# Performance work log

Measured on AMD Instinct MI355X. Metric: run time of the kernel, lower is better.

Reference implementation:

```python
import jax, jax.numpy as jnp
import numpy as np

ITEMNUM = 50000
NUM_HEADS = 4
EPS = 1e-8


def _ln(x, g, b):
    m = x.mean(-1, keepdims=True)
    v = ((x - m) ** 2).mean(-1, keepdims=True)
    return (x - m) * jax.lax.rsqrt(v + EPS) * g + b


def _forward(seqs_data, position, seqs, time_emb, pos_table, gate_W, gate_b,
             ln_attn_g, ln_attn_b, qW, qb, kW, kb, vW, vb,
             ln_ffn_g, ln_ffn_b, c1W, c1b, c2W, c2b, last_g, last_b):
    B, L, H = seqs.shape
    nb = qW.shape[0]
    hd = H // NUM_HEADS

    pe = pos_table[position]                      # [B,L,H]
    seqs = seqs + pe
    time = time_emb + pe
    # per-position per-block time gates, [B,L,nb]
    gates = jax.nn.sigmoid(jnp.einsum('blh,nh->bln', time, gate_W) + gate_b)

    keep = (seqs_data != ITEMNUM - 1)[..., None].astype(seqs.dtype)  # [B,L,1]
    seqs = seqs * keep
    tril = jnp.tril(jnp.ones((L, L), dtype=bool))  # causal: keep lower triangle
    neg_inf = jnp.asarray(-jnp.inf, seqs.dtype)
    scale = 1.0 / np.sqrt(hd).astype(np.float32)

    for i in range(nb):
        Q = _ln(seqs, ln_attn_g[i], ln_attn_b[i])
        q = Q @ qW[i].T + qb[i]
        k = time @ kW[i].T + kb[i]
        v = (seqs + time) @ vW[i].T + vb[i]
        # [B,nh,L,hd]
        q = q.reshape(B, L, NUM_HEADS, hd).transpose(0, 2, 1, 3)
        k = k.reshape(B, L, NUM_HEADS, hd).transpose(0, 2, 1, 3)
        v = v.reshape(B, L, NUM_HEADS, hd).transpose(0, 2, 1, 3)
        scores = jnp.einsum('bhqd,bhkd->bhqk', q, k) * scale  # [B,nh,L,L]
        tg = gates[:, :, i]                                   # [B,L]
        gate_mat = tg[:, None, :, None] * tg[:, None, None, :]  # [B,1,L,L] outer product
        scores = jnp.where(tril[None, None], scores * gate_mat, neg_inf)
        attn = jax.nn.softmax(scores, axis=-1)
        out = jnp.einsum('bhqk,bhkd->bhqd', attn, v)
        out = out.transpose(0, 2, 1, 3).reshape(B, L, H)
        x = Q + out
        x = _ln(x, ln_ffn_g[i], ln_ffn_b[i])
        # PointWiseFeedForward: two 1x1 convs == two linears, relu, residual
        h = jax.nn.relu(x @ c1W[i].T + c1b[i])
        seqs = (h @ c2W[i].T + c2b[i] + x) * keep

    return _ln(seqs, last_g, last_b)


def setup_inputs() -> dict:
    key = jax.random.key(0)
    B, L, H, NB, ML = 64, 512, 256, 2, 512
    ks = iter(jax.random.split(key, 32))
    nrm = lambda shape, s=0.05: jax.random.normal(next(ks), shape, jnp.float32) * s
    pos_table = nrm((ML, H), 0.02).at[0].set(0.0)  # padding_idx=0
    inp = {
        'seqs_data': jax.random.randint(next(ks), (B, L), 0, ITEMNUM - 1, jnp.int32),
        'seqs': nrm((B, L, H), 1.0),
        'position': jax.random.randint(next(ks), (B, L), 0, ML, jnp.int32),
        'time_emb': nrm((B, L, H), 1.0),
        'pos_table': pos_table,
        'gate_W': nrm((NB, H)), 'gate_b': jnp.zeros((NB,), jnp.float32),
        'ln_attn_g': jnp.ones((NB, H), jnp.float32), 'ln_attn_b': jnp.zeros((NB, H), jnp.float32),
        'qW': nrm((NB, H, H)), 'qb': jnp.zeros((NB, H), jnp.float32),
        'kW': nrm((NB, H, H)), 'kb': jnp.zeros((NB, H), jnp.float32),
        'vW': nrm((NB, H, H)), 'vb': jnp.zeros((NB, H), jnp.float32),
        'ln_ffn_g': jnp.ones((NB, H), jnp.float32), 'ln_ffn_b': jnp.zeros((NB, H), jnp.float32),
        'c1W': nrm((NB, H, H)), 'c1b': jnp.zeros((NB, H), jnp.float32),
        'c2W': nrm((NB, H, H)), 'c2b': jnp.zeros((NB, H), jnp.float32),
        'last_g': jnp.ones((H,), jnp.float32), 'last_b': jnp.zeros((H,), jnp.float32),
    }
    return inp


def reference(seqs_data, seqs, position, time_emb, pos_table, gate_W, gate_b,
              ln_attn_g, ln_attn_b, qW, qb, kW, kb, vW, vb,
              ln_ffn_g, ln_ffn_b, c1W, c1b, c2W, c2b, last_g, last_b):
    return _forward(seqs_data, position, seqs, time_emb, pos_table, gate_W, gate_b,
                    ln_attn_g, ln_attn_b, qW, qb, kW, kb, vW, vb,
                    ln_ffn_g, ln_ffn_b, c1W, c1b, c2W, c2b, last_g, last_b)
```

## Files before the change

### kernel.cpp

```cpp
#include <hip/hip_runtime.h>
#include <hip/hip_bf16.h>
#include <math.h>

#define NTOK 32768
#define Hdim 256
#define Ldim 512
#define Bdim 64
#define NHEAD 4
#define HD 64
#define PADV 49999

typedef __bf16 bf16x8 __attribute__((ext_vector_type(8)));
typedef __bf16 bf16x4 __attribute__((ext_vector_type(4)));
typedef float  f32x4  __attribute__((ext_vector_type(4)));
typedef unsigned short u16x8 __attribute__((ext_vector_type(8)));

union bf8u { bf16x8 v8; bf16x4 v4[2]; };

__device__ __forceinline__ unsigned short f2bf(float f) {
    unsigned int u = __float_as_uint(f);
    unsigned int r = (u + 0x7fffu + ((u >> 16) & 1u)) >> 16;
    return (unsigned short)r;
}
__device__ __forceinline__ float bf2f(unsigned short u) {
    return __uint_as_float(((unsigned int)u) << 16);
}

__device__ __forceinline__ void gload16(const void* g, void* l) {
    __builtin_amdgcn_global_load_lds((const __attribute__((address_space(1))) unsigned int*)g,
                                     (__attribute__((address_space(3))) unsigned int*)l,
                                     16, 0, 0);
}

__global__ __launch_bounds__(256)
void castw_kernel(const float* __restrict__ q, const float* __restrict__ k,
                  const float* __restrict__ v, const float* __restrict__ c1,
                  const float* __restrict__ c2, unsigned short* __restrict__ dst) {
    const float* srcs[5] = {q, k, v, c1, c2};
    const float* s = srcs[blockIdx.y];
    int idx = blockIdx.x * 1024 + threadIdx.x * 4;
    float4 f = *(const float4*)(s + idx);
    unsigned short* d = dst + (size_t)blockIdx.y * 131072 + idx;
    d[0] = f2bf(f.x); d[1] = f2bf(f.y); d[2] = f2bf(f.z); d[3] = f2bf(f.w);
}

__global__ __launch_bounds__(256)
void prep_ln_kernel(const int* __restrict__ seqs_data, const float* __restrict__ seqs,
                    const int* __restrict__ position, const float* __restrict__ time_emb,
                    const float* __restrict__ pos_table, const float* __restrict__ gate_W,
                    const float* __restrict__ gate_b,
                    const float* __restrict__ lnG, const float* __restrict__ lnB,
                    unsigned short* __restrict__ Tbf,
                    unsigned short* __restrict__ QXbf,
                    unsigned short* __restrict__ VINbf,
                    float* __restrict__ gates, float* __restrict__ keepv) {
    int tok  = blockIdx.x * 4 + (threadIdx.x >> 6);
    int lane = threadIdx.x & 63;
    size_t off = (size_t)tok * Hdim + lane * 4;
    int pos = position[tok];
    float4 pe = *(const float4*)(pos_table + (size_t)pos * Hdim + lane * 4);
    float4 sq = *(const float4*)(seqs + off);
    float4 tm = *(const float4*)(time_emb + off);
    float keep = (seqs_data[tok] != PADV) ? 1.0f : 0.0f;
    float4 t = {tm.x + pe.x, tm.y + pe.y, tm.z + pe.z, tm.w + pe.w};
    float4 s = {(sq.x + pe.x) * keep, (sq.y + pe.y) * keep,
                (sq.z + pe.z) * keep, (sq.w + pe.w) * keep};
    ushort4 tb = {f2bf(t.x), f2bf(t.y), f2bf(t.z), f2bf(t.w)};
    *(ushort4*)(Tbf + off) = tb;
    float4 gw0 = *(const float4*)(gate_W + lane * 4);
    float4 gw1 = *(const float4*)(gate_W + Hdim + lane * 4);
    float r0 = s.x + s.y + s.z + s.w;
    float r1 = s.x * s.x + s.y * s.y + s.z * s.z + s.w * s.w;
    float r2 = t.x * gw0.x + t.y * gw0.y + t.z * gw0.z + t.w * gw0.w;
    float r3 = t.x * gw1.x + t.y * gw1.y + t.z * gw1.z + t.w * gw1.w;
#pragma unroll
    for (int o = 1; o < 64; o <<= 1) {
        r0 += __shfl_xor(r0, o, 64);
        r1 += __shfl_xor(r1, o, 64);
        r2 += __shfl_xor(r2, o, 64);
        r3 += __shfl_xor(r3, o, 64);
    }
    float mean = r0 * (1.0f / Hdim);
    float var  = fmaxf(r1 * (1.0f / Hdim) - mean * mean, 0.0f);
    float rstd = rsqrtf(var + 1e-8f);
    if (lane == 0) {
        gates[(size_t)tok * 2 + 0] = 1.0f / (1.0f + __expf(-(r2 + gate_b[0])));
        gates[(size_t)tok * 2 + 1] = 1.0f / (1.0f + __expf(-(r3 + gate_b[1])));
        keepv[tok] = keep;
    }
    float4 g4 = *(const float4*)(lnG + lane * 4);
    float4 b4 = *(const float4*)(lnB + lane * 4);
    float4 y = {(s.x - mean) * rstd * g4.x + b4.x, (s.y - mean) * rstd * g4.y + b4.y,
                (s.z - mean) * rstd * g4.z + b4.z, (s.w - mean) * rstd * g4.w + b4.w};
    ushort4 yb = {f2bf(y.x), f2bf(y.y), f2bf(y.z), f2bf(y.w)};
    *(ushort4*)(QXbf + off) = yb;
    ushort4 vb = {f2bf(s.x + t.x), f2bf(s.y + t.y), f2bf(s.z + t.z), f2bf(s.w + t.w)};
    *(ushort4*)(VINbf + off) = vb;
}

#define GBM 128
#define GBN 128
#define GBK 64

__device__ __forceinline__ void stage64(const unsigned short* __restrict__ src,
                                        size_t rowBase, __bf16* lds, int tid, int kc) {
#pragma unroll
    for (int it = 0; it < 4; ++it) {
        int c = tid + it * 256;
        int r = c >> 3, sub = c & 7;
        int g = sub ^ (r & 7);
        gload16(src + (rowBase + r) * Hdim + kc + g * 8, lds + c * 8);
    }
}
__device__ __forceinline__ bf16x8 frag64(const __bf16* lds, int r, int g) {
    return *(const bf16x8*)(lds + r * 64 + (g ^ (r & 7)) * 8);
}

__global__ __launch_bounds__(256)
void gemm_qkv_kernel(const unsigned short* __restrict__ QXbf,
                     const unsigned short* __restrict__ Tbf,
                     const unsigned short* __restrict__ VINbf,
                     const unsigned short* __restrict__ qW,
                     const unsigned short* __restrict__ kW,
                     const unsigned short* __restrict__ vW,
                     const float* __restrict__ qb, const float* __restrict__ kb,
                     const float* __restrict__ vb,
                     unsigned short* __restrict__ Qbf,
                     unsigned short* __restrict__ Kbf,
                     unsigned short* __restrict__ VT) {
    __shared__ __align__(16) char smem[128 * 136 * 2];
    __bf16* As = (__bf16*)smem;
    __bf16* Ws = (__bf16*)(smem + 16384);
    __bf16 (*Ct)[136] = (__bf16 (*)[136])smem;
    int z = blockIdx.z;
    const unsigned short* A = (z == 0) ? QXbf : (z == 1) ? Tbf : VINbf;
    const unsigned short* W = (z == 0) ? qW : (z == 1) ? kW : vW;
    const float* bias       = (z == 0) ? qb : (z == 1) ? kb : vb;

    int tid = threadIdx.x, lane = tid & 63, w = tid >> 6;
    int wr = w >> 1, wc = w & 1;
    int m0 = blockIdx.y * GBM, n0 = blockIdx.x * GBN;
    f32x4 acc[4][4];
#pragma unroll
    for (int i = 0; i < 4; ++i)
#pragma unroll
        for (int j = 0; j < 4; ++j) acc[i][j] = (f32x4)(0.0f);
    int colq = lane & 15, kg = lane >> 4;
    for (int kc = 0; kc < Hdim; kc += GBK) {
        __syncthreads();
        stage64(A, m0, As, tid, kc);
        stage64(W, n0, Ws, tid, kc);
        __syncthreads();
        bf16x8 af[4][2], bfr[4][2];
#pragma unroll
        for (int i = 0; i < 4; ++i) {
            int r = wr * 64 + i * 16 + colq;
            af[i][0] = frag64(As, r, kg);
            af[i][1] = frag64(As, r, 4 + kg);
        }
#pragma unroll
        for (int j = 0; j < 4; ++j) {
            int r = wc * 64 + j * 16 + colq;
            bfr[j][0] = frag64(Ws, r, kg);
            bfr[j][1] = frag64(Ws, r, 4 + kg);
        }
#pragma unroll
        for (int i = 0; i < 4; ++i)
#pragma unroll
            for (int j = 0; j < 4; ++j) {
                acc[i][j] = __builtin_amdgcn_mfma_f32_16x16x32_bf16(af[i][0], bfr[j][0], acc[i][j], 0, 0, 0);
                acc[i][j] = __builtin_amdgcn_mfma_f32_16x16x32_bf16(af[i][1], bfr[j][1], acc[i][j], 0, 0, 0);
            }
    }
    int rowq = (lane >> 4) * 4;
    if (z < 2) {
        unsigned short* outBF = (z == 0) ? Qbf : Kbf;
#pragma unroll
        for (int i = 0; i < 4; ++i)
#pragma unroll
            for (int r = 0; r < 4; ++r) {
                int m = m0 + wr * 64 + i * 16 + rowq + r;
#pragma unroll
                for (int j = 0; j < 4; ++j) {
                    int n = n0 + wc * 64 + j * 16 + colq;
                    outBF[(size_t)m * Hdim + n] = f2bf(acc[i][j][r] + bias[n]);
                }
            }
    } else {
        __syncthreads();
#pragma unroll
        for (int i = 0; i < 4; ++i)
#pragma unroll
            for (int r = 0; r < 4; ++r) {
                int ml = wr * 64 + i * 16 + rowq + r;
#pragma unroll
                for (int j = 0; j < 4; ++j) {
                    int nl = wc * 64 + j * 16 + colq;
                    Ct[nl][ml] = (__bf16)(acc[i][j][r] + bias[n0 + nl]);
                }
            }
        __syncthreads();
        int bb = m0 >> 9, l0 = m0 & 511;
#pragma unroll
        for (int it = 0; it < 8; ++it) {
            int c = tid + it * 256;
            int nl = c >> 4;
            int o8 = (c & 15) * 8;
            int n = n0 + nl;
            int hh = n >> 6, dd = n & 63;
            bf16x8 v = *(const bf16x8*)&Ct[nl][o8];
            *(bf16x8*)(VT + ((((size_t)bb * NHEAD + hh) * HD + dd) * Ldim + l0 + o8)) = v;
        }
    }
}

#define FFN_LDS (65536 + 32768)

__device__ __forceinline__ int swz(int r, int g) {
    return (g & 24) | ((g & 7) ^ (r & 7));
}

__device__ __forceinline__ void ffn_gemm(const unsigned short* __restrict__ W,
                                         const __bf16* Abuf, __bf16* Wst,
                                         int tid, int wr, int wc, int colq, int kg,
                                         f32x4 acc[4][4]) {
#pragma unroll
    for (int i = 0; i < 4; ++i)
#pragma unroll
        for (int j = 0; j < 4; ++j) acc[i][j] = (f32x4)(0.0f);
    for (int kc = 0; kc < Hdim; kc += 64) {
        __syncthreads();
#pragma unroll
        for (int it = 0; it < 4; ++it) {
            int c = tid + it * 512;
            int r = c >> 3, sub = c & 7;
            int g = sub ^ (r & 7);
            gload16(W + (size_t)r * Hdim + kc + g * 8, Wst + c * 8);
        }
        __syncthreads();
        bf16x8 af[4][2], bfr[4][2];
#pragma unroll
        for (int i = 0; i < 4; ++i) {
            int r = wr * 64 + i * 16 + colq;
            af[i][0] = *(const bf16x8*)(Abuf + r * 256 + kc + ((kg) ^ (r & 7)) * 8);
            af[i][1] = *(const bf16x8*)(Abuf + r * 256 + kc + ((4 + kg) ^ (r & 7)) * 8);
        }
#pragma unroll
        for (int j = 0; j < 4; ++j) {
            int n = wc * 64 + j * 16 + colq;
            bfr[j][0] = frag64(Wst, n, kg);
            bfr[j][1] = frag64(Wst, n, 4 + kg);
        }
#pragma unroll
        for (int i = 0; i < 4; ++i)
#pragma unroll
            for (int j = 0; j < 4; ++j) {
                acc[i][j] = __builtin_amdgcn_mfma_f32_16x16x32_bf16(af[i][0], bfr[j][0], acc[i][j], 0, 0, 0);
                acc[i][j] = __builtin_amdgcn_mfma_f32_16x16x32_bf16(af[i][1], bfr[j][1], acc[i][j], 0, 0, 0);
            }
    }
}

__global__ __launch_bounds__(512, 1)
void ffn_kernel(const unsigned short* __restrict__ Qx,
                const unsigned short* __restrict__ Qa,
                const float* __restrict__ lnG, const float* __restrict__ lnB,
                const unsigned short* __restrict__ c1Wb, const float* __restrict__ c1b,
                const unsigned short* __restrict__ c2Wb, const float* __restrict__ c2b,
                const float* __restrict__ keepv,
                const unsigned short* __restrict__ Tbf,
                const float* __restrict__ oG, const float* __restrict__ oB,
                float* __restrict__ outF,
                unsigned short* __restrict__ QxOut,
                unsigned short* __restrict__ VINout) {
    extern __shared__ __align__(16) char smem[];
    __bf16* Abuf   = (__bf16*)smem;
    __bf16* Wst    = (__bf16*)(smem + 65536);
    float*  statsF = (float*)(smem + 65536);

    int m0  = blockIdx.x * 128;
    int tid = threadIdx.x, lane = tid & 63, w = tid >> 6;
    int wr = w >> 2, wc = w & 3;
    int colq = lane & 15, kg = lane >> 4;
    int rowq = (lane >> 4) * 4;

    float xc[8][8];
#pragma unroll
    for (int it = 0; it < 8; ++it) {
        int c = tid + it * 512;
        int r = c >> 5, g = c & 31;
        size_t off = (size_t)(m0 + r) * Hdim + g * 8;
        u16x8 qv = *(const u16x8*)(Qx + off);
        u16x8 av = *(const u16x8*)(Qa + off);
        float cs = 0.0f, cq = 0.0f;
#pragma unroll
        for (int j = 0; j < 8; ++j) {
            float x = bf2f(qv[j]) + bf2f(av[j]);
            xc[it][j] = x;
            cs += x; cq += x * x;
        }
#pragma unroll
        for (int o = 1; o < 32; o <<= 1) {
            cs += __shfl_xor(cs, o, 32);
            cq += __shfl_xor(cq, o, 32);
        }
        if ((tid & 31) == 0) { statsF[r * 2] = cs; statsF[r * 2 + 1] = cq; }
    }
    __syncthreads();
    u16x8 xnreg[8];
#pragma unroll
    for (int it = 0; it < 8; ++it) {
        int c = tid + it * 512;
        int r = c >> 5, g = c & 31, col = g * 8;
        float mean = statsF[r * 2] * (1.0f / Hdim);
        float var  = fmaxf(statsF[r * 2 + 1] * (1.0f / Hdim) - mean * mean, 0.0f);
        float rstd = rsqrtf(var + 1e-8f);
        float4 g0 = *(const float4*)(lnG + col), g1 = *(const float4*)(lnG + col + 4);
        float4 b0 = *(const float4*)(lnB + col), b1 = *(const float4*)(lnB + col + 4);
        float gv[8] = {g0.x, g0.y, g0.z, g0.w, g1.x, g1.y, g1.z, g1.w};
        float bv[8] = {b0.x, b0.y, b0.z, b0.w, b1.x, b1.y, b1.z, b1.w};
        u16x8 xn;
#pragma unroll
        for (int j = 0; j < 8; ++j)
            xn[j] = f2bf((xc[it][j] - mean) * rstd * gv[j] + bv[j]);
        xnreg[it] = xn;
        *(u16x8*)(Abuf + r * 256 + swz(r, g) * 8) = xn;
    }

    f32x4 acc[4][4];
    ffn_gemm(c1Wb, Abuf, Wst, tid, wr, wc, colq, kg, acc);
    float bj[4];
#pragma unroll
    for (int j = 0; j < 4; ++j) bj[j] = c1b[wc * 64 + j * 16 + colq];
    __syncthreads();
#pragma unroll
    for (int i = 0; i < 4; ++i)
#pragma unroll
        for (int r = 0; r < 4; ++r) {
            int m = wr * 64 + i * 16 + rowq + r;
#pragma unroll
            for (int j = 0; j < 4; ++j) {
                int n = wc * 64 + j * 16 + colq;
                float v = fmaxf(acc[i][j][r] + bj[j], 0.0f);
                Abuf[m * 256 + swz(m, n >> 3) * 8 + (n & 7)] = (__bf16)v;
            }
        }

    ffn_gemm(c2Wb, Abuf, Wst, tid, wr, wc, colq, kg, acc);
#pragma unroll
    for (int j = 0; j < 4; ++j) bj[j] = c2b[wc * 64 + j * 16 + colq];
    __syncthreads();
#pragma unroll
    for (int i = 0; i < 4; ++i)
#pragma unroll
        for (int r = 0; r < 4; ++r) {
            int m = wr * 64 + i * 16 + rowq + r;
#pragma unroll
            for (int j = 0; j < 4; ++j) {
                int n = wc * 64 + j * 16 + colq;
                Abuf[m * 256 + swz(m, n >> 3) * 8 + (n & 7)] = (__bf16)(acc[i][j][r] + bj[j]);
            }
        }
    __syncthreads();

    float sc[8][8];
#pragma unroll
    for (int it = 0; it < 8; ++it) {
        int c = tid + it * 512;
        int r = c >> 5, g = c & 31;
        u16x8 zv = *(const u16x8*)(Abuf + r * 256 + swz(r, g) * 8);
        u16x8 xn = xnreg[it];
        float kf = keepv[m0 + r];
        float cs = 0.0f, cq = 0.0f;
#pragma unroll
        for (int j = 0; j < 8; ++j) {
            float s = (bf2f(zv[j]) + bf2f(xn[j])) * kf;
            sc[it][j] = s;
            cs += s; cq += s * s;
        }
#pragma unroll
        for (int o = 1; o < 32; o <<= 1) {
            cs += __shfl_xor(cs, o, 32);
            cq += __shfl_xor(cq, o, 32);
        }
        if ((tid & 31) == 0) { statsF[r * 2] = cs; statsF[r * 2 + 1] = cq; }
    }
    __syncthreads();
#pragma unroll
    for (int it = 0; it < 8; ++it) {
        int c = tid + it * 512;
        int r = c >> 5, g = c & 31, col = g * 8;
        float mean = statsF[r * 2] * (1.0f / Hdim);
        float var  = fmaxf(statsF[r * 2 + 1] * (1.0f / Hdim) - mean * mean, 0.0f);
        float rstd = rsqrtf(var + 1e-8f);
        float4 g0 = *(const float4*)(oG + col), g1 = *(const float4*)(oG + col + 4);
        float4 b0 = *(const float4*)(oB + col), b1 = *(const float4*)(oB + col + 4);
        float gv[8] = {g0.x, g0.y, g0.z, g0.w, g1.x, g1.y, g1.z, g1.w};
        float bv[8] = {b0.x, b0.y, b0.z, b0.w, b1.x, b1.y, b1.z, b1.w};
        size_t off = (size_t)(m0 + r) * Hdim + col;
        float y[8];
#pragma unroll
        for (int j = 0; j < 8; ++j)
            y[j] = (sc[it][j] - mean) * rstd * gv[j] + bv[j];
        if (outF) {
            float4 o0 = {y[0], y[1], y[2], y[3]};
            float4 o1 = {y[4], y[5], y[6], y[7]};
            *(float4*)(outF + off)     = o0;
            *(float4*)(outF + off + 4) = o1;
        } else {
            u16x8 yb, vb;
            u16x8 tv = *(const u16x8*)(Tbf + off);
#pragma unroll
            for (int j = 0; j < 8; ++j) {
                yb[j] = f2bf(y[j]);
                vb[j] = f2bf(sc[it][j] + bf2f(tv[j]));
            }
            *(u16x8*)(QxOut + off)  = yb;
            *(u16x8*)(VINout + off) = vb;
        }
    }
}

#define AKS 68
#define AVS 516
#define APS 68
#define ATTN_LDS (512 * AKS * 2 + 64 * AVS * 2 + 192 * APS * 2)
__global__ __launch_bounds__(768, 1)
void attn_mfma_kernel(const unsigned short* __restrict__ Qg,
                      const unsigned short* __restrict__ Kg,
                      const unsigned short* __restrict__ VTg,
                      const float* __restrict__ gates,
                      unsigned short* __restrict__ Ob, int blk) {
    extern __shared__ __align__(16) char smem[];
    __bf16 (*Ks)[AKS]  = (__bf16 (*)[AKS])smem;
    __bf16 (*VTs)[AVS] = (__bf16 (*)[AVS])(smem + 512 * AKS * 2);
    __bf16 (*Ps)[APS]  = (__bf16 (*)[APS])(smem + 512 * AKS * 2 + 64 * AVS * 2);
    int h = blockIdx.x & 3, b = blockIdx.x >> 2;
    int tid = threadIdx.x, lane = tid & 63, w = tid >> 6;
    int colq = lane & 15, grp = lane >> 4;
    int rowq = grp * 4, kq = grp * 8;

    size_t baseK = (size_t)b * Ldim * Hdim + h * HD;
    for (int c = tid; c < 4096; c += 768) {
        int r = c >> 3, o = (c & 7) * 8;
        bf8u u;
        u.v8 = *(const bf16x8*)(Kg + baseK + (size_t)r * Hdim + o);
        *(bf16x4*)&Ks[r][o]     = u.v4[0];
        *(bf16x4*)&Ks[r][o + 4] = u.v4[1];
    }
    size_t baseV = ((size_t)b * NHEAD + h) * HD * Ldim;
    for (int c = tid; c < 4096; c += 768) {
        int d = c >> 6, k = (c & 63) * 8;
        bf8u u;
        u.v8 = *(const bf16x8*)(VTg + baseV + (size_t)d * Ldim + k);
        *(bf16x4*)&VTs[d][k]     = u.v4[0];
        *(bf16x4*)&VTs[d][k + 4] = u.v4[1];
    }
    __syncthreads();

    const float lscale = 0.125f * 1.44269504f;
    int gl[3], ng;
    if (w < 4)      { gl[0] = w;     gl[1] = 8 + w;  gl[2] = 28 + w; ng = 3; }
    else if (w < 8) { gl[0] = w;     gl[1] = 8 + w;  gl[2] = 16 + w; ng = 3; }
    else            { gl[0] = 8 + w; gl[1] = 16 + w; gl[2] = 0;      ng = 2; }

    for (int gi = 0; gi < ng; ++gi) {
        int g = gl[gi];
        int q0 = g * 16;
        size_t qrow = (size_t)(b * Ldim + q0 + colq) * Hdim + h * HD;
        bf16x8 afq0 = *(const bf16x8*)(Qg + qrow + kq);
        bf16x8 afq1 = *(const bf16x8*)(Qg + qrow + 32 + kq);
        float gql[4];
#pragma unroll
        for (int r = 0; r < 4; ++r)
            gql[r] = gates[((size_t)b * Ldim + q0 + rowq + r) * 2 + blk] * lscale;

        float lrun[4] = {0.0f, 0.0f, 0.0f, 0.0f};
        f32x4 accO[4];
#pragma unroll
        for (int jd = 0; jd < 4; ++jd) accO[jd] = (f32x4)(0.0f);

        int nfull = g >> 2;
        for (int kt = 0; kt <= nfull; ++kt) {
            int k0 = kt * 64;
            bool diag = (kt == nfull);
            f32x4 sv[4];
#pragma unroll
            for (int j = 0; j < 4; ++j) sv[j] = (f32x4)(0.0f);
#pragma unroll
            for (int j = 0; j < 4; ++j) {
                int kr = k0 + j * 16 + colq;
                bf8u b0, b1;
                b0.v4[0] = *(const bf16x4*)&Ks[kr][kq];
                b0.v4[1] = *(const bf16x4*)&Ks[kr][kq + 4];
                b1.v4[0] = *(const bf16x4*)&Ks[kr][32 + kq];
                b1.v4[1] = *(const bf16x4*)&Ks[kr][32 + kq + 4];
                sv[j] = __builtin_amdgcn_mfma_f32_16x16x32_bf16(afq0, b0.v8, sv[j], 0, 0, 0);
                sv[j] = __builtin_amdgcn_mfma_f32_16x16x32_bf16(afq1, b1.v8, sv[j], 0, 0, 0);
            }
            float gkv[4];
#pragma unroll
            for (int j = 0; j < 4; ++j)
                gkv[j] = gates[((size_t)b * Ldim + k0 + j * 16 + colq) * 2 + blk];
#pragma unroll
            for (int r = 0; r < 4; ++r) {
                float su = 0.0f;
                float p4[4];
                if (diag) {
                    int qg = q0 + rowq + r;
#pragma unroll
                    for (int j = 0; j < 4; ++j) {
                        float v = sv[j][r] * gql[r] * gkv[j];
                        v = (k0 + j * 16 + colq > qg) ? -1e38f : v;
                        float e = exp2f(v);
                        p4[j] = e;
                        su += e;
                    }
                } else {
#pragma unroll
                    for (int j = 0; j < 4; ++j) {
                        float e = exp2f(sv[j][r] * gql[r] * gkv[j]);
                        p4[j] = e;
                        su += e;
                    }
                }
#pragma unroll
                for (int off = 1; off < 16; off <<= 1)
                    su += __shfl_xor(su, off, 16);
                lrun[r] += su;
#pragma unroll
                for (int j = 0; j < 4; ++j)
                    Ps[w * 16 + rowq + r][j * 16 + colq] = (__bf16)p4[j];
            }
            bf8u a0, a1;
            a0.v4[0] = *(const bf16x4*)&Ps[w * 16 + colq][kq];
            a0.v4[1] = *(const bf16x4*)&Ps[w * 16 + colq][kq + 4];
            a1.v4[0] = *(const bf16x4*)&Ps[w * 16 + colq][32 + kq];
            a1.v4[1] = *(const bf16x4*)&Ps[w * 16 + colq][32 + kq + 4];
#pragma unroll
            for (int jd = 0; jd < 4; ++jd) {
                int vr = jd * 16 + colq;
                bf8u v0, v1;
                v0.v4[0] = *(const bf16x4*)&VTs[vr][k0 + kq];
                v0.v4[1] = *(const bf16x4*)&VTs[vr][k0 + kq + 4];
                v1.v4[0] = *(const bf16x4*)&VTs[vr][k0 + 32 + kq];
                v1.v4[1] = *(const bf16x4*)&VTs[vr][k0 + 32 + kq + 4];
                accO[jd] = __builtin_amdgcn_mfma_f32_16x16x32_bf16(a0.v8, v0.v8, accO[jd], 0, 0, 0);
                accO[jd] = __builtin_amdgcn_mfma_f32_16x16x32_bf16(a1.v8, v1.v8, accO[jd], 0, 0, 0);
            }
        }
#pragma unroll
        for (int r = 0; r < 4; ++r) {
            float inv = 1.0f / lrun[r];
#pragma unroll
            for (int jd = 0; jd < 4; ++jd)
                Ob[(size_t)(b * Ldim + q0 + rowq + r) * Hdim + h * HD + jd * 16 + colq] =
                    f2bf(accO[jd][r] * inv);
        }
    }
}

extern "C" void kernel_launch(void* const* d_in, const int* in_sizes, int n_in,
                              void* d_out, int out_size, void* d_ws, size_t ws_size,
                              hipStream_t stream) {
    const int*   seqs_data = (const int*)d_in[0];
    const float* seqs      = (const float*)d_in[1];
    const int*   position  = (const int*)d_in[2];
    const float* time_emb  = (const float*)d_in[3];
    const float* pos_table = (const float*)d_in[4];
    const float* gate_W    = (const float*)d_in[5];
    const float* gate_b    = (const float*)d_in[6];
    const float* ln_attn_g = (const float*)d_in[7];
    const float* ln_attn_b = (const float*)d_in[8];
    const float* qW        = (const float*)d_in[9];
    const float* qb        = (const float*)d_in[10];
    const float* kW        = (const float*)d_in[11];
    const float* kb        = (const float*)d_in[12];
    const float* vW        = (const float*)d_in[13];
    const float* vb        = (const float*)d_in[14];
    const float* ln_ffn_g  = (const float*)d_in[15];
    const float* ln_ffn_b  = (const float*)d_in[16];
    const float* c1W       = (const float*)d_in[17];
    const float* c1b       = (const float*)d_in[18];
    const float* c2W       = (const float*)d_in[19];
    const float* c2b       = (const float*)d_in[20];
    const float* last_g    = (const float*)d_in[21];
    const float* last_b    = (const float*)d_in[22];

    size_t BUF = (size_t)NTOK * Hdim;
    float* fws = (float*)d_ws;
    float* GATES = fws;
    float* KEEP  = GATES + (size_t)NTOK * 2;
    unsigned short* bws   = (unsigned short*)(KEEP + NTOK);
    unsigned short* Tbf   = bws;
    unsigned short* QXbf  = Tbf + BUF;
    unsigned short* VINbf = QXbf + BUF;
    unsigned short* HIDbf = VINbf + BUF;
    unsigned short* Qbf   = HIDbf + BUF;
    unsigned short* Kbf   = Qbf + BUF;
    unsigned short* VTbf  = Kbf + BUF;
    unsigned short* QAbf  = VTbf + BUF;
    unsigned short* Zbf   = QAbf + BUF;
    unsigned short* Wbf   = Zbf + BUF;
    size_t WB = (size_t)Hdim * Hdim;
    unsigned short* qWbf  = Wbf;
    unsigned short* kWbf  = Wbf + 2 * WB;
    unsigned short* vWbf  = Wbf + 4 * WB;
    unsigned short* c1Wbf = Wbf + 6 * WB;
    unsigned short* c2Wbf = Wbf + 8 * WB;

    castw_kernel<<<dim3(128, 5), 256, 0, stream>>>(qW, kW, vW, c1W, c2W, Wbf);
    prep_ln_kernel<<<NTOK / 4, 256, 0, stream>>>(seqs_data, seqs, position, time_emb,
                                                 pos_table, gate_W, gate_b,
                                                 ln_attn_g, ln_attn_b,
                                                 Tbf, QXbf, VINbf, GATES, KEEP);

    dim3 qkvgrid(Hdim / GBN, NTOK / GBM, 3);
    for (int i = 0; i < 2; ++i) {
        gemm_qkv_kernel<<<qkvgrid, 256, 0, stream>>>(QXbf, Tbf, VINbf,
                                                     qWbf + i * WB, kWbf + i * WB, vWbf + i * WB,
                                                     qb + i * Hdim, kb + i * Hdim, vb + i * Hdim,
                                                     Qbf, Kbf, VTbf);
        attn_mfma_kernel<<<Bdim * NHEAD, 768, ATTN_LDS, stream>>>(Qbf, Kbf, VTbf, GATES, QAbf, i);
        ffn_kernel<<<NTOK / 128, 512, FFN_LDS, stream>>>(
            QXbf, QAbf,
            ln_ffn_g + i * Hdim, ln_ffn_b + i * Hdim,
            c1Wbf + i * WB, c1b + i * Hdim,
            c2Wbf + i * WB, c2b + i * Hdim,
            KEEP, Tbf,
            (i == 0) ? ln_attn_g + Hdim : last_g,
            (i == 0) ? ln_attn_b + Hdim : last_b,
            (i == 0) ? nullptr : (float*)d_out,
            QXbf, VINbf);
    }
}
```

Measured before the change: 354.1 us.

## Shrink FFN tile to 64 rows, prefetch next weight chunk during MFMA

The FFN kernel now handles 64 rows per block with 256 threads and asks for two blocks per CU, cutting LDS to about 64KB so two blocks can share a CU. Weight staging is restructured so the next 64-column weight chunk is loaded right after the current fragments are read, overlapping global loads with the MFMA work. The c2 weights are prefetched before the first GEMM's epilogue. Register arrays of float activations are replaced by packed bf16 registers that are recomputed when needed, to lower register pressure at the cost of some extra conversions. The aim is more occupancy and less stalling on weight loads, but smaller tiles mean each weight chunk is reused across fewer rows.

```diff
diff --git a/kernel.cpp b/kernel.cpp
--- a/kernel.cpp
+++ b/kernel.cpp
@@ -214,15 +214,27 @@
     }
 }
 
-#define FFN_LDS (65536 + 32768)
+#define FBM 64
+#define FFN_LDS (32768 + 32768 + 512)
 
 __device__ __forceinline__ int swz(int r, int g) {
     return (g & 24) | ((g & 7) ^ (r & 7));
 }
 
+__device__ __forceinline__ void ffn_stage(const unsigned short* __restrict__ W, int kc,
+                                          __bf16* Wst, int tid) {
+#pragma unroll
+    for (int it = 0; it < 8; ++it) {
+        int c = tid + it * 256;
+        int r = c >> 3, sub = c & 7;
+        int g = sub ^ (r & 7);
+        gload16(W + (size_t)r * Hdim + kc + g * 8, Wst + c * 8);
+    }
+}
+
 __device__ __forceinline__ void ffn_gemm(const unsigned short* __restrict__ W,
                                          const __bf16* Abuf, __bf16* Wst,
-                                         int tid, int wr, int wc, int colq, int kg,
+                                         int tid, int w, int colq, int kg,
                                          f32x4 acc[4][4]) {
 #pragma unroll
     for (int i = 0; i < 4; ++i)
@@ -230,27 +242,21 @@
         for (int j = 0; j < 4; ++j) acc[i][j] = (f32x4)(0.0f);
     for (int kc = 0; kc < Hdim; kc += 64) {
         __syncthreads();
-#pragma unroll
-        for (int it = 0; it < 4; ++it) {
-            int c = tid + it * 512;
-            int r = c >> 3, sub = c & 7;
-            int g = sub ^ (r & 7);
-            gload16(W + (size_t)r * Hdim + kc + g * 8, Wst + c * 8);
-        }
-        __syncthreads();
         bf16x8 af[4][2], bfr[4][2];
 #pragma unroll
         for (int i = 0; i < 4; ++i) {
-            int r = wr * 64 + i * 16 + colq;
-            af[i][0] = *(const bf16x8*)(Abuf + r * 256 + kc + ((kg) ^ (r & 7)) * 8);
-            af[i][1] = *(const bf16x8*)(Abuf + r * 256 + kc + ((4 + kg) ^ (r & 7)) * 8);
+            int r = i * 16 + colq;
+            af[i][0] = *(const bf16x8*)(Abuf + r * 256 + ((kc >> 3) | (kg ^ (r & 7))) * 8);
+            af[i][1] = *(const bf16x8*)(Abuf + r * 256 + ((kc >> 3) | ((4 + kg) ^ (r & 7))) * 8);
         }
 #pragma unroll
         for (int j = 0; j < 4; ++j) {
-            int n = wc * 64 + j * 16 + colq;
+            int n = w * 64 + j * 16 + colq;
             bfr[j][0] = frag64(Wst, n, kg);
             bfr[j][1] = frag64(Wst, n, 4 + kg);
         }
+        __syncthreads();
+        if (kc < Hdim - 64) ffn_stage(W, kc + 64, Wst, tid);
 #pragma unroll
         for (int i = 0; i < 4; ++i)
 #pragma unroll
@@ -261,7 +267,7 @@
     }
 }
 
-__global__ __launch_bounds__(512, 1)
+__global__ __launch_bounds__(256, 2)
 void ffn_kernel(const unsigned short* __restrict__ Qx,
                 const unsigned short* __restrict__ Qa,
                 const float* __restrict__ lnG, const float* __restrict__ lnB,
@@ -275,28 +281,33 @@
                 unsigned short* __restrict__ VINout) {
     extern __shared__ __align__(16) char smem[];
     __bf16* Abuf   = (__bf16*)smem;
-    __bf16* Wst    = (__bf16*)(smem + 65536);
+    __bf16* Wst    = (__bf16*)(smem + 32768);
     float*  statsF = (float*)(smem + 65536);
 
-    int m0  = blockIdx.x * 128;
+    int m0  = blockIdx.x * FBM;
     int tid = threadIdx.x, lane = tid & 63, w = tid >> 6;
-    int wr = w >> 2, wc = w & 3;
     int colq = lane & 15, kg = lane >> 4;
-    int rowq = (lane >> 4) * 4;
-
-    float xc[8][8];
+    int rowq = kg * 4;
+
+    ffn_stage(c1Wb, 0, Wst, tid);
+
+    u16x8 qvr[8], avr[8];
 #pragma unroll
     for (int it = 0; it < 8; ++it) {
-        int c = tid + it * 512;
+        int c = tid + it * 256;
         int r = c >> 5, g = c & 31;
         size_t off = (size_t)(m0 + r) * Hdim + g * 8;
-        u16x8 qv = *(const u16x8*)(Qx + off);
-        u16x8 av = *(const u16x8*)(Qa + off);
+        qvr[it] = *(const u16x8*)(Qx + off);
+        avr[it] = *(const u16x8*)(Qa + off);
+    }
+#pragma unroll
+    for (int it = 0; it < 8; ++it) {
+        int c = tid + it * 256;
+        int r = c >> 5;
         float cs = 0.0f, cq = 0.0f;
 #pragma unroll
         for (int j = 0; j < 8; ++j) {
-            float x = bf2f(qv[j]) + bf2f(av[j]);
-            xc[it][j] = x;
+            float x = bf2f(qvr[it][j]) + bf2f(avr[it][j]);
             cs += x; cq += x * x;
         }
 #pragma unroll
@@ -310,7 +321,7 @@
     u16x8 xnreg[8];
 #pragma unroll
     for (int it = 0; it < 8; ++it) {
-        int c = tid + it * 512;
+        int c = tid + it * 256;
         int r = c >> 5, g = c & 31, col = g * 8;
         float mean = statsF[r * 2] * (1.0f / Hdim);
         float var  = fmaxf(statsF[r * 2 + 1] * (1.0f / Hdim) - mean * mean, 0.0f);
@@ -321,61 +332,65 @@
         float bv[8] = {b0.x, b0.y, b0.z, b0.w, b1.x, b1.y, b1.z, b1.w};
         u16x8 xn;
 #pragma unroll
-        for (int j = 0; j < 8; ++j)
-            xn[j] = f2bf((xc[it][j] - mean) * rstd * gv[j] + bv[j]);
+        for (int j = 0; j < 8; ++j) {
+            float x = bf2f(qvr[it][j]) + bf2f(avr[it][j]);
+            xn[j] = f2bf((x - mean) * rstd * gv[j] + bv[j]);
+        }
         xnreg[it] = xn;
         *(u16x8*)(Abuf + r * 256 + swz(r, g) * 8) = xn;
     }
 
     f32x4 acc[4][4];
-    ffn_gemm(c1Wb, Abuf, Wst, tid, wr, wc, colq, kg, acc);
+    ffn_gemm(c1Wb, Abuf, Wst, tid, w, colq, kg, acc);
+    ffn_stage(c2Wb, 0, Wst, tid);
     float bj[4];
 #pragma unroll
-    for (int j = 0; j < 4; ++j) bj[j] = c1b[wc * 64 + j * 16 + colq];
-    __syncthreads();
+    for (int j = 0; j < 4; ++j) bj[j] = c1b[w * 64 + j * 16 + colq];
 #pragma unroll
     for (int i = 0; i < 4; ++i)
 #pragma unroll
         for (int r = 0; r < 4; ++r) {
-            int m = wr * 64 + i * 16 + rowq + r;
+            int m = i * 16 + rowq + r;
 #pragma unroll
             for (int j = 0; j < 4; ++j) {
-                int n = wc * 64 + j * 16 + colq;
+                int n = w * 64 + j * 16 + colq;
                 float v = fmaxf(acc[i][j][r] + bj[j], 0.0f);
                 Abuf[m * 256 + swz(m, n >> 3) * 8 + (n & 7)] = (__bf16)v;
             }
         }
 
-    ffn_gemm(c2Wb, Abuf, Wst, tid, wr, wc, colq, kg, acc);
-#pragma unroll
-    for (int j = 0; j < 4; ++j) bj[j] = c2b[wc * 64 + j * 16 + colq];
+    ffn_gemm(c2Wb, Abuf, Wst, tid, w, colq, kg, acc);
+#pragma unroll
+    for (int j = 0; j < 4; ++j) bj[j] = c2b[w * 64 + j * 16 + colq];
+#pragma unroll
+    for (int i = 0; i < 4; ++i)
+#pragma unroll
+        for (int r = 0; r < 4; ++r) {
+            int m = i * 16 + rowq + r;
+#pragma unroll
+            for (int j = 0; j < 4; ++j) {
+                int n = w * 64 + j * 16 + colq;
+                Abuf[m * 256 + swz(m, n >> 3) * 8 + (n & 7)] = (__bf16)(acc[i][j][r] + bj[j]);
+            }
+        }
     __syncthreads();
-#pragma unroll
-    for (int i = 0; i < 4; ++i)
-#pragma unroll
-        for (int r = 0; r < 4; ++r) {
-            int m = wr * 64 + i * 16 + rowq + r;
-#pragma unroll
-            for (int j = 0; j < 4; ++j) {
-                int n = wc * 64 + j * 16 + colq;
-                Abuf[m * 256 + swz(m, n >> 3) * 8 + (n & 7)] = (__bf16)(acc[i][j][r] + bj[j]);
-            }
-        }
-    __syncthreads();
-
-    float sc[8][8];
+
+    u16x8 zvr[8];
 #pragma unroll
     for (int it = 0; it < 8; ++it) {
-        int c = tid + it * 512;
+        int c = tid + it * 256;
         int r = c >> 5, g = c & 31;
-        u16x8 zv = *(const u16x8*)(Abuf + r * 256 + swz(r, g) * 8);
-        u16x8 xn = xnreg[it];
+        zvr[it] = *(const u16x8*)(Abuf + r * 256 + swz(r, g) * 8);
+    }
+#pragma unroll
+    for (int it = 0; it < 8; ++it) {
+        int c = tid + it * 256;
+        int r = c >> 5;
         float kf = keepv[m0 + r];
         float cs = 0.0f, cq = 0.0f;
 #pragma unroll
         for (int j = 0; j < 8; ++j) {
-            float s = (bf2f(zv[j]) + bf2f(xn[j])) * kf;
-            sc[it][j] = s;
+            float s = (bf2f(zvr[it][j]) + bf2f(xnreg[it][j])) * kf;
             cs += s; cq += s * s;
         }
 #pragma unroll
@@ -388,8 +403,9 @@
     __syncthreads();
 #pragma unroll
     for (int it = 0; it < 8; ++it) {
-        int c = tid + it * 512;
+        int c = tid + it * 256;
         int r = c >> 5, g = c & 31, col = g * 8;
+        float kf = keepv[m0 + r];
         float mean = statsF[r * 2] * (1.0f / Hdim);
         float var  = fmaxf(statsF[r * 2 + 1] * (1.0f / Hdim) - mean * mean, 0.0f);
         float rstd = rsqrtf(var + 1e-8f);
@@ -398,10 +414,12 @@
         float gv[8] = {g0.x, g0.y, g0.z, g0.w, g1.x, g1.y, g1.z, g1.w};
         float bv[8] = {b0.x, b0.y, b0.z, b0.w, b1.x, b1.y, b1.z, b1.w};
         size_t off = (size_t)(m0 + r) * Hdim + col;
-        float y[8];
-#pragma unroll
-        for (int j = 0; j < 8; ++j)
-            y[j] = (sc[it][j] - mean) * rstd * gv[j] + bv[j];
+        float y[8], sv[8];
+#pragma unroll
+        for (int j = 0; j < 8; ++j) {
+            sv[j] = (bf2f(zvr[it][j]) + bf2f(xnreg[it][j])) * kf;
+            y[j] = (sv[j] - mean) * rstd * gv[j] + bv[j];
+        }
         if (outF) {
             float4 o0 = {y[0], y[1], y[2], y[3]};
             float4 o1 = {y[4], y[5], y[6], y[7]};
@@ -413,7 +431,7 @@
 #pragma unroll
             for (int j = 0; j < 8; ++j) {
                 yb[j] = f2bf(y[j]);
-                vb[j] = f2bf(sc[it][j] + bf2f(tv[j]));
+                vb[j] = f2bf(sv[j] + bf2f(tv[j]));
             }
             *(u16x8*)(QxOut + off)  = yb;
             *(u16x8*)(VINout + off) = vb;
@@ -622,7 +640,7 @@
                                                      qb + i * Hdim, kb + i * Hdim, vb + i * Hdim,
                                                      Qbf, Kbf, VTbf);
         attn_mfma_kernel<<<Bdim * NHEAD, 768, ATTN_LDS, stream>>>(Qbf, Kbf, VTbf, GATES, QAbf, i);
-        ffn_kernel<<<NTOK / 128, 512, FFN_LDS, stream>>>(
+        ffn_kernel<<<NTOK / FBM, 256, FFN_LDS, stream>>>(
             QXbf, QAbf,
             ln_ffn_g + i * Hdim, ln_ffn_b + i * Hdim,
             c1Wbf + i * WB, c1b + i * Hdim,
```

New measurement: 357.3 us. No clear change (+0.9%).
